# Kernel optimization log

Measured on AMD Instinct MI355X. Metric: run time of the kernel, lower is better.

Reference implementation:

```python
import jax, jax.numpy as jnp
import numpy as np

EPS = 1e-5
GROUPS = 8


def setup_inputs() -> dict:
    key = jax.random.key(0)
    ks = jax.random.split(key, 6)
    C = 512
    B, H, W = 4, 64, 64
    s = 1.0 / np.sqrt(C)
    return {
        "x": jax.random.normal(ks[0], (B, C, H, W), dtype=jnp.float32),
        "gn_gamma": jnp.ones((C,), jnp.float32),
        "gn_beta": jnp.zeros((C,), jnp.float32),
        "wq": jax.random.normal(ks[1], (C, C), jnp.float32) * s,
        "bq": jnp.zeros((C,), jnp.float32),
        "wk": jax.random.normal(ks[2], (C, C), jnp.float32) * s,
        "bk": jnp.zeros((C,), jnp.float32),
        "wv": jax.random.normal(ks[3], (C, C), jnp.float32) * s,
        "bv": jnp.zeros((C,), jnp.float32),
        "wp": jax.random.normal(ks[4], (C, C), jnp.float32) * s,
        "bp": jnp.zeros((C,), jnp.float32),
    }


def _group_norm(x, gamma, beta):
    b, c, h, w = x.shape
    xg = x.reshape(b, GROUPS, c // GROUPS, h, w)
    mu = xg.mean(axis=(2, 3, 4), keepdims=True)
    var = xg.var(axis=(2, 3, 4), keepdims=True)
    xn = ((xg - mu) * jax.lax.rsqrt(var + EPS)).reshape(b, c, h, w)
    return xn * gamma[None, :, None, None] + beta[None, :, None, None]


def _conv1x1(x, w, b):
    # 1x1 conv == channel-mixing matmul: [O,C] x [B,C,H,W] -> [B,O,H,W]
    return jnp.einsum('oc,bchw->bohw', w, x) + b[None, :, None, None]


def reference(x, gn_gamma, gn_beta, wq, bq, wk, bk, wv, bv, wp, bp):
    b, c, h, w = x.shape
    xn = _group_norm(x, gn_gamma, gn_beta)  # note: residual uses normalized x, as in source
    q = _conv1x1(xn, wq, bq).reshape(b, c, h * w)
    k = _conv1x1(xn, wk, bk).reshape(b, c, h * w)
    v = _conv1x1(xn, wv, bv).reshape(b, c, h * w)
    scale = jnp.asarray(c, x.dtype) ** 0.5
    attn = jnp.einsum('bci,bcj->bij', q, k) / scale  # [b, hw, hw]
    attn = jax.nn.softmax(attn, axis=2)
    out = jnp.einsum('bij,bcj->bci', attn, v).reshape(b, c, h, w)
    out = _conv1x1(out, wp, bp)
    return xn + out
```

## Files before the change

kernel.cpp:

```cpp
#include <hip/hip_runtime.h>
#include <hip/hip_bf16.h>


typedef unsigned short u16;
typedef unsigned char u8;
typedef __bf16 bf16x8 __attribute__((ext_vector_type(8)));
typedef float f32x4 __attribute__((ext_vector_type(4)));
typedef int i32x4 __attribute__((ext_vector_type(4)));
typedef int i32x8 __attribute__((ext_vector_type(8)));
typedef unsigned short u16x4 __attribute__((ext_vector_type(4)));
typedef unsigned short u16x8 __attribute__((ext_vector_type(8)));

#define CDIM 512
#define NPOS 4096
#define NBATCH 4

__device__ __forceinline__ u16 f2bf(float x) {
  union { float f; unsigned u; } c; c.f = x;
  unsigned u = c.u;
  u += 0x7fffu + ((u >> 16) & 1u);
  return (u16)(u >> 16);
}
__device__ __forceinline__ float bf2f(u16 h) {
  union { unsigned u; float f; } c; c.u = ((unsigned)h) << 16;
  return c.f;
}
__device__ __forceinline__ unsigned pk4_fp8(float a, float b, float c, float d) {
  unsigned v = __builtin_amdgcn_cvt_pk_fp8_f32(a, b, 0, false);
  v = __builtin_amdgcn_cvt_pk_fp8_f32(c, d, v, true);
  return v;
}

__device__ __forceinline__ void async16(const u16* g, u16* l) {
  __builtin_amdgcn_global_load_lds(
      (const __attribute__((address_space(1))) unsigned int*)g,
      (__attribute__((address_space(3))) unsigned int*)l, 16, 0, 0);
}
__device__ __forceinline__ void async16b(const u8* g, u8* l) {
  __builtin_amdgcn_global_load_lds(
      (const __attribute__((address_space(1))) unsigned int*)g,
      (__attribute__((address_space(3))) unsigned int*)l, 16, 0, 0);
}

__device__ __forceinline__ float wred_sum(float v) {
#pragma unroll
  for (int o = 32; o > 0; o >>= 1) v += __shfl_xor(v, o, 64);
  return v;
}

__global__ __launch_bounds__(256) void gn_partial(const float* __restrict__ x,
                                                  float* __restrict__ stats) {
  int gidx = blockIdx.x >> 3;
  int slice = blockIdx.x & 7;
  const float4* src = (const float4*)x + (long)gidx * 65536 + (long)slice * 8192;
  float s = 0.f, ss = 0.f;
  for (int i = threadIdx.x; i < 8192; i += 256) {
    float4 v = src[i];
    s  += v.x + v.y + v.z + v.w;
    ss += v.x * v.x + v.y * v.y + v.z * v.z + v.w * v.w;
  }
  s = wred_sum(s); ss = wred_sum(ss);
  __shared__ float r1[4], r2[4];
  int lane = threadIdx.x & 63, wave = threadIdx.x >> 6;
  if (lane == 0) { r1[wave] = s; r2[wave] = ss; }
  __syncthreads();
  if (threadIdx.x == 0) {
    atomicAdd(&stats[gidx * 2 + 0], r1[0] + r1[1] + r1[2] + r1[3]);
    atomicAdd(&stats[gidx * 2 + 1], r2[0] + r2[1] + r2[2] + r2[3]);
  }
}

__global__ __launch_bounds__(256) void norm_trans(const float* __restrict__ x,
                                                  const float* __restrict__ stats,
                                                  const float* __restrict__ gamma,
                                                  const float* __restrict__ beta,
                                                  u16* __restrict__ xnb,
                                                  u16* __restrict__ xnT) {
  __shared__ float tile[32][33];
  int b = blockIdx.z, c0 = blockIdx.y * 32, p0 = blockIdx.x * 32;
  int g = (b << 3) + (c0 >> 6);
  float cnt = 1.f / 262144.f;
  float mu = stats[g * 2 + 0] * cnt;
  float ms = stats[g * 2 + 1] * cnt;
  float rstd = rsqrtf(ms - mu * mu + 1e-5f);
  int tp = threadIdx.x & 31, tc = threadIdx.x >> 5;
#pragma unroll
  for (int r = 0; r < 4; r++) {
    int cl = tc + r * 8;
    int c = c0 + cl;
    long idx = ((long)(b * CDIM + c)) * NPOS + p0 + tp;
    float v = (x[idx] - mu) * rstd * gamma[c] + beta[c];
    xnb[idx] = f2bf(v);
    tile[cl][tp] = v;
  }
  __syncthreads();
#pragma unroll
  for (int r = 0; r < 4; r++) {
    int pl = tc + r * 8, cl = tp;
    xnT[((long)(b * NPOS + p0 + pl)) * CDIM + c0 + cl] = f2bf(tile[cl][pl]);
  }
}

__global__ __launch_bounds__(256) void cvt4(const float* __restrict__ a, const float* __restrict__ b,
                                            const float* __restrict__ c, const float* __restrict__ d,
                                            u16* __restrict__ oa, u16* __restrict__ ob,
                                            u16* __restrict__ oc, u16* __restrict__ od) {
  int i = blockIdx.x * 256 + threadIdx.x;
  if (blockIdx.y == 3) {
    int m = i >> 9, k = i & 511;
    u16 v = f2bf(d[i]);
    od[m * 1024 + k] = v;
    od[m * 1024 + 512 + k] = v;
    return;
  }
  const float* src; u16* dst;
  switch (blockIdx.y) {
    case 0: src = a; dst = oa; break;
    case 1: src = b; dst = ob; break;
    default: src = c; dst = oc; break;
  }
  dst[i] = f2bf(src[i]);
}

template <int MODE, int BN>
__global__ __launch_bounds__(BN * 2, 4) void gemm_bt(
    const u16* __restrict__ A, const u16* __restrict__ B,
    void* __restrict__ Cp, const float* __restrict__ bias,
    const float* __restrict__ bias1, const u16* __restrict__ residb,
    const float* __restrict__ laux,
    int N, int K, int lda, int ldb,
    long sA, long sB, long sC, long sR) {
  __shared__ u16 Asm[128 * 64];
  __shared__ u16 Bsm[BN * 64];
  constexpr int NT = BN * 2;
  constexpr int STEP = NT / 8;
  int bz = blockIdx.z;
  A += (long)bz * sA;
  B += (long)bz * sB;
  int bm = blockIdx.y, bn = blockIdx.x;
  int tid = threadIdx.x;
  int lane = tid & 63, wave = tid >> 6;
  int wm = (wave & 1) * 64, wn = (wave >> 1) * 64;

  int row0 = tid >> 3;
  int ko = (tid & 7) * 8;
  int kos = ko ^ ((row0 & 7) * 8);
  f32x4 acc[4][4] = {};
  int row16 = lane & 15;
  int kq = (lane >> 4) * 8;

  for (int k0 = 0; k0 < K; k0 += 64) {
#pragma unroll
    for (int r = 0; r < 128 / STEP; r++) {
      int row = row0 + r * STEP;
      async16(A + (long)(bm * 128 + row) * lda + k0 + kos, &Asm[row * 64 + ko]);
    }
#pragma unroll
    for (int r = 0; r < BN / STEP; r++) {
      int row = row0 + r * STEP;
      async16(B + (long)(bn * BN + row) * ldb + k0 + kos, &Bsm[row * 64 + ko]);
    }
    __syncthreads();
#pragma unroll
    for (int s2 = 0; s2 < 2; s2++) {
      bf16x8 af[4], bfr[4];
#pragma unroll
      for (int i = 0; i < 4; i++) {
        int row = wm + i * 16 + row16;
        af[i] = *(const bf16x8*)&Asm[row * 64 + ((s2 * 32 + kq) ^ ((row & 7) * 8))];
      }
#pragma unroll
      for (int j = 0; j < 4; j++) {
        int row = wn + j * 16 + row16;
        bfr[j] = *(const bf16x8*)&Bsm[row * 64 + ((s2 * 32 + kq) ^ ((row & 7) * 8))];
      }
#pragma unroll
      for (int i = 0; i < 4; i++)
#pragma unroll
        for (int j = 0; j < 4; j++)
          acc[i][j] = __builtin_amdgcn_mfma_f32_16x16x32_bf16(bfr[j], af[i], acc[i][j], 0, 0, 0);
    }
    __syncthreads();
  }

  int mcol = lane & 15, rb = (lane >> 4) * 4;
  long zC = (long)bz * sC;
#pragma unroll
  for (int i = 0; i < 4; i++) {
    int gm = bm * 128 + wm + i * 16 + mcol;
    float bm_add = 0.f;
    if constexpr (MODE == 4 || MODE == 5) bm_add = bias[gm];
#pragma unroll
    for (int j = 0; j < 4; j++) {
      int gn0 = bn * BN + wn + j * 16 + rb;
      long off = zC + (long)gm * N + gn0;
      float v[4];
#pragma unroll
      for (int r = 0; r < 4; r++) v[r] = acc[i][j][r];
      if constexpr (MODE == 0) {
        const float* bb = (gn0 < 512) ? (bias + gn0) : (bias1 + (gn0 - 512));
#pragma unroll
        for (int r = 0; r < 4; r++) v[r] += bb[r];
        *(unsigned*)&((u8*)Cp)[off] = pk4_fp8(v[0], v[1], v[2], v[3]);
      }
      if constexpr (MODE == 4) {
        f32x4 lv = *(const f32x4*)&laux[bz * NPOS + gn0];
        u16x4 rv = *(const u16x4*)&residb[(long)bz * sR + (long)gm * N + gn0];
        f32x4 o;
#pragma unroll
        for (int r = 0; r < 4; r++) o[r] = v[r] / lv[r] + bm_add + bf2f(rv[r]);
        *(f32x4*)&((float*)Cp)[off] = o;
      }
      if constexpr (MODE == 5) {
#pragma unroll
        for (int r = 0; r < 4; r++) v[r] += bm_add;
        *(unsigned*)&((u8*)Cp)[off] = pk4_fp8(v[0], v[1], v[2], v[3]);
      }
    }
  }
}

__global__ __launch_bounds__(256, 3) void smx_gemm(const u8* __restrict__ QKf8,
                                                   u8* __restrict__ P,
                                                   float* __restrict__ l,
                                                   float scale) {
  __shared__ u8 Asm[128 * 128];
  __shared__ u8 Bsm[128 * 128];
  int bz = blockIdx.z;
  const u8* Ab = QKf8 + (long)bz * 4194304;
  const u8* Bb = Ab + 512;
  int bm = blockIdx.y, bn = blockIdx.x;
  int tid = threadIdx.x, lane = tid & 63, wave = tid >> 6;
  int wm = (wave & 1) * 64, wn = (wave >> 1) * 64;
  int m16 = lane & 15, q = lane >> 4;
  int lrow8 = lane >> 3, lch = lane & 7;

  f32x4 acc[4][4] = {};

  for (int k0 = 0; k0 < 512; k0 += 128) {
#pragma unroll
    for (int r = 0; r < 4; r++) {
      int row = (wave * 4 + r) * 8 + lrow8;
      int ch = lch ^ (row & 7);
      async16b(Ab + (long)(bm * 128 + row) * 1024 + k0 + ch * 16, &Asm[row * 128 + lch * 16]);
      async16b(Bb + (long)(bn * 128 + row) * 1024 + k0 + ch * 16, &Bsm[row * 128 + lch * 16]);
    }
    __syncthreads();
    i32x8 af[4], bf[4];
#pragma unroll
    for (int i = 0; i < 4; i++) {
      int row = wm + i * 16 + m16;
      int sw = (row & 7) * 16;
      i32x4 lo = *(const i32x4*)&Asm[row * 128 + ((q * 32) ^ sw)];
      i32x4 hi = *(const i32x4*)&Asm[row * 128 + ((q * 32 + 16) ^ sw)];
      af[i] = __builtin_shufflevector(lo, hi, 0, 1, 2, 3, 4, 5, 6, 7);
    }
#pragma unroll
    for (int j = 0; j < 4; j++) {
      int row = wn + j * 16 + m16;
      int sw = (row & 7) * 16;
      i32x4 lo = *(const i32x4*)&Bsm[row * 128 + ((q * 32) ^ sw)];
      i32x4 hi = *(const i32x4*)&Bsm[row * 128 + ((q * 32 + 16) ^ sw)];
      bf[j] = __builtin_shufflevector(lo, hi, 0, 1, 2, 3, 4, 5, 6, 7);
    }
#pragma unroll
    for (int i = 0; i < 4; i++)
#pragma unroll
      for (int j = 0; j < 4; j++)
        acc[i][j] = __builtin_amdgcn_mfma_scale_f32_16x16x128_f8f6f4(
            bf[j], af[i], acc[i][j], 0, 0, 0, 0x7F7F7F7F, 0, 0x7F7F7F7F);
    __syncthreads();
  }

  long zC = (long)bz * 16777216;
  float rsum[4] = {0.f, 0.f, 0.f, 0.f};
#pragma unroll
  for (int i = 0; i < 4; i++) {
    int gi = bm * 128 + wm + i * 16 + m16;
#pragma unroll
    for (int j = 0; j < 4; j++) {
      int gj = bn * 128 + wn + j * 16 + q * 4;
      float v[4];
#pragma unroll
      for (int r = 0; r < 4; r++) { v[r] = __expf(acc[i][j][r] * scale); rsum[i] += v[r]; }
      *(unsigned*)&P[zC + (long)gi * 4096 + gj] = pk4_fp8(v[0], v[1], v[2], v[3]);
    }
  }
#pragma unroll
  for (int i = 0; i < 4; i++) {
    rsum[i] += __shfl_xor(rsum[i], 16, 64);
    rsum[i] += __shfl_xor(rsum[i], 32, 64);
  }
  if (lane < 16) {
    int base = bz * NPOS + bm * 128 + wm + m16;
#pragma unroll
    for (int i = 0; i < 4; i++)
      atomicAdd(&l[base + i * 16], rsum[i]);
  }
}

__global__ __launch_bounds__(256, 3) void hgemm_mx(const u8* __restrict__ P,
                                                   const u8* __restrict__ V,
                                                   u16* __restrict__ part) {
  __shared__ u8 Asm[128 * 128];
  __shared__ u8 Bsm[128 * 128];
  int z = blockIdx.z;
  int bz = z >> 1, sp = z & 1;
  const u8* Ab = P + (long)bz * 16777216 + sp * 2048;
  const u8* Bb = V + (long)bz * 2097152 + sp * 2048;
  int bm = blockIdx.y, bn = blockIdx.x;
  int tid = threadIdx.x, lane = tid & 63, wave = tid >> 6;
  int wm = (wave & 1) * 64, wn = (wave >> 1) * 64;
  int m16 = lane & 15, q = lane >> 4;
  int lrow8 = lane >> 3, lch = lane & 7;

  f32x4 acc[4][4] = {};

  for (int k0 = 0; k0 < 2048; k0 += 128) {
#pragma unroll
    for (int r = 0; r < 4; r++) {
      int row = (wave * 4 + r) * 8 + lrow8;
      int ch = lch ^ (row & 7);
      async16b(Ab + (long)(bm * 128 + row) * 4096 + k0 + ch * 16, &Asm[row * 128 + lch * 16]);
      async16b(Bb + (long)(bn * 128 + row) * 4096 + k0 + ch * 16, &Bsm[row * 128 + lch * 16]);
    }
    __syncthreads();
    i32x8 af[4], bf[4];
#pragma unroll
    for (int i = 0; i < 4; i++) {
      int row = wm + i * 16 + m16;
      int sw = (row & 7) * 16;
      i32x4 lo = *(const i32x4*)&Asm[row * 128 + ((q * 32) ^ sw)];
      i32x4 hi = *(const i32x4*)&Asm[row * 128 + ((q * 32 + 16) ^ sw)];
      af[i] = __builtin_shufflevector(lo, hi, 0, 1, 2, 3, 4, 5, 6, 7);
    }
#pragma unroll
    for (int j = 0; j < 4; j++) {
      int row = wn + j * 16 + m16;
      int sw = (row & 7) * 16;
      i32x4 lo = *(const i32x4*)&Bsm[row * 128 + ((q * 32) ^ sw)];
      i32x4 hi = *(const i32x4*)&Bsm[row * 128 + ((q * 32 + 16) ^ sw)];
      bf[j] = __builtin_shufflevector(lo, hi, 0, 1, 2, 3, 4, 5, 6, 7);
    }
#pragma unroll
    for (int i = 0; i < 4; i++)
#pragma unroll
      for (int j = 0; j < 4; j++)
        acc[i][j] = __builtin_amdgcn_mfma_scale_f32_16x16x128_f8f6f4(
            bf[j], af[i], acc[i][j], 0, 0, 0, 0x7F7F7F7F, 0, 0x7F7F7F7F);
    __syncthreads();
  }

  long zC = (long)bz * 4194304 + sp * 512;
#pragma unroll
  for (int i = 0; i < 4; i++) {
    int gi = bm * 128 + wm + i * 16 + m16;
#pragma unroll
    for (int j = 0; j < 4; j++) {
      int gc = bn * 128 + wn + j * 16 + q * 4;
      u16x4 o;
#pragma unroll
      for (int r = 0; r < 4; r++) o[r] = f2bf(acc[i][j][r]);
      *(u16x4*)&part[zC + (long)gi * 1024 + gc] = o;
    }
  }
}

extern "C" void kernel_launch(void* const* d_in, const int* in_sizes, int n_in,
                              void* d_out, int out_size, void* d_ws, size_t ws_size,
                              hipStream_t stream) {
  const float* x     = (const float*)d_in[0];
  const float* gamma = (const float*)d_in[1];
  const float* beta  = (const float*)d_in[2];
  const float* wq = (const float*)d_in[3];
  const float* bq = (const float*)d_in[4];
  const float* wk = (const float*)d_in[5];
  const float* bk = (const float*)d_in[6];
  const float* wv = (const float*)d_in[7];
  const float* bv = (const float*)d_in[8];
  const float* wp = (const float*)d_in[9];
  const float* bp = (const float*)d_in[10];
  float* out = (float*)d_out;

  char* W = (char*)d_ws;
  float* stats = (float*)(W + 0);
  float* l     = (float*)(W + 256);
  u16* xnb  = (u16*)(W + 65792);
  u16* xnT  = (u16*)(W + 16843008);
  u16* wqkb = (u16*)(W + 33620224);
  u16* wvb  = (u16*)(W + 34668800);
  u16* wpd  = (u16*)(W + 35193088);
  u8*  QKf8 = (u8*)(W + 37290240);
  u8*  Vf8  = (u8*)(W + 54067456);
  u16* part = (u16*)(W + 62456064);
  u8*  SP   = (u8*)(W + 96010496);
  (void)in_sizes; (void)n_in; (void)out_size; (void)ws_size;

  hipMemsetAsync(W, 0, 65792, stream);
  gn_partial<<<256, 256, 0, stream>>>(x, stats);
  norm_trans<<<dim3(128, 16, 4), 256, 0, stream>>>(x, stats, gamma, beta, xnb, xnT);
  cvt4<<<dim3(1024, 4), 256, 0, stream>>>(wq, wk, wv, wp, wqkb, wqkb + 262144, wvb, wpd);

  const long NC = (long)NPOS * CDIM;
  const long CN = (long)CDIM * NPOS;
  const long QKS = (long)NPOS * 1024;
  const float scale = 0.044194173824159216f;

  gemm_bt<0, 256><<<dim3(4, 128, 1), 512, 0, stream>>>(xnT, wqkb, QKf8, bq, bk, nullptr, nullptr,
      1024, CDIM, CDIM, CDIM, 0, 0, 0, 0);
  gemm_bt<5, 128><<<dim3(32, 4, 4), 256, 0, stream>>>(wvb, xnT, Vf8, bv, nullptr, nullptr, nullptr,
      NPOS, CDIM, CDIM, CDIM, 0, NC, CN, 0);
  smx_gemm<<<dim3(32, 32, NBATCH), 256, 0, stream>>>(QKf8, SP, l, scale);
  hgemm_mx<<<dim3(4, 32, 8), 256, 0, stream>>>(SP, Vf8, part);
  gemm_bt<4, 128><<<dim3(32, 4, 4), 256, 0, stream>>>(wpd, part, (void*)out, bp, nullptr, xnb, l,
      NPOS, 1024, 1024, 1024, 0, (long)NPOS * 1024, CN, CN);
}
```

Baseline: 326.9 us.

## Double-buffer LDS tiles in all GEMM kernels with prefetch and MFMA priority

Converts the bf16 gemm_bt, the fp8 score GEMM and the PV GEMM to double-buffered LDS. The next K tile is issued asynchronously before computing on the current one, and each step ends with an explicit vmcnt drain plus barrier. MFMA sections are wrapped in s_setprio to favour math issue. The QK projection launch also switches from a 256-wide tile to a 128-wide tile. Doubling LDS lowers the occupancy hint from 3-4 to 2 blocks per CU, which may reduce latency hiding.

```diff
diff --git a/kernel.cpp b/kernel.cpp
--- a/kernel.cpp
+++ b/kernel.cpp
@@ -40,6 +40,11 @@
   __builtin_amdgcn_global_load_lds(
       (const __attribute__((address_space(1))) unsigned int*)g,
       (__attribute__((address_space(3))) unsigned int*)l, 16, 0, 0);
+}
+
+__device__ __forceinline__ void drain_barrier() {
+  asm volatile("s_waitcnt vmcnt(0)" ::: "memory");
+  __builtin_amdgcn_s_barrier();
 }
 
 __device__ __forceinline__ float wred_sum(float v) {
@@ -123,15 +128,15 @@
 }
 
 template <int MODE, int BN>
-__global__ __launch_bounds__(BN * 2, 4) void gemm_bt(
+__global__ __launch_bounds__(BN * 2, 2) void gemm_bt(
     const u16* __restrict__ A, const u16* __restrict__ B,
     void* __restrict__ Cp, const float* __restrict__ bias,
     const float* __restrict__ bias1, const u16* __restrict__ residb,
     const float* __restrict__ laux,
     int N, int K, int lda, int ldb,
     long sA, long sB, long sC, long sR) {
-  __shared__ u16 Asm[128 * 64];
-  __shared__ u16 Bsm[BN * 64];
+  __shared__ u16 Asm[2][128 * 64];
+  __shared__ u16 Bsm[2][BN * 64];
   constexpr int NT = BN * 2;
   constexpr int STEP = NT / 8;
   int bz = blockIdx.z;
@@ -149,38 +154,47 @@
   int row16 = lane & 15;
   int kq = (lane >> 4) * 8;
 
-  for (int k0 = 0; k0 < K; k0 += 64) {
+  auto stage = [&](int buf, int k0) {
 #pragma unroll
     for (int r = 0; r < 128 / STEP; r++) {
       int row = row0 + r * STEP;
-      async16(A + (long)(bm * 128 + row) * lda + k0 + kos, &Asm[row * 64 + ko]);
+      async16(A + (long)(bm * 128 + row) * lda + k0 + kos, &Asm[buf][row * 64 + ko]);
     }
 #pragma unroll
     for (int r = 0; r < BN / STEP; r++) {
       int row = row0 + r * STEP;
-      async16(B + (long)(bn * BN + row) * ldb + k0 + kos, &Bsm[row * 64 + ko]);
-    }
-    __syncthreads();
+      async16(B + (long)(bn * BN + row) * ldb + k0 + kos, &Bsm[buf][row * 64 + ko]);
+    }
+  };
+
+  stage(0, 0);
+  drain_barrier();
+  int cur = 0;
+  for (int k0 = 0; k0 < K; k0 += 64) {
+    if (k0 + 64 < K) stage(cur ^ 1, k0 + 64);
 #pragma unroll
     for (int s2 = 0; s2 < 2; s2++) {
       bf16x8 af[4], bfr[4];
 #pragma unroll
       for (int i = 0; i < 4; i++) {
         int row = wm + i * 16 + row16;
-        af[i] = *(const bf16x8*)&Asm[row * 64 + ((s2 * 32 + kq) ^ ((row & 7) * 8))];
+        af[i] = *(const bf16x8*)&Asm[cur][row * 64 + ((s2 * 32 + kq) ^ ((row & 7) * 8))];
       }
 #pragma unroll
       for (int j = 0; j < 4; j++) {
         int row = wn + j * 16 + row16;
-        bfr[j] = *(const bf16x8*)&Bsm[row * 64 + ((s2 * 32 + kq) ^ ((row & 7) * 8))];
+        bfr[j] = *(const bf16x8*)&Bsm[cur][row * 64 + ((s2 * 32 + kq) ^ ((row & 7) * 8))];
       }
+      __builtin_amdgcn_s_setprio(1);
 #pragma unroll
       for (int i = 0; i < 4; i++)
 #pragma unroll
         for (int j = 0; j < 4; j++)
           acc[i][j] = __builtin_amdgcn_mfma_f32_16x16x32_bf16(bfr[j], af[i], acc[i][j], 0, 0, 0);
-    }
-    __syncthreads();
+      __builtin_amdgcn_s_setprio(0);
+    }
+    drain_barrier();
+    cur ^= 1;
   }
 
   int mcol = lane & 15, rb = (lane >> 4) * 4;
@@ -220,12 +234,12 @@
   }
 }
 
-__global__ __launch_bounds__(256, 3) void smx_gemm(const u8* __restrict__ QKf8,
+__global__ __launch_bounds__(256, 2) void smx_gemm(const u8* __restrict__ QKf8,
                                                    u8* __restrict__ P,
                                                    float* __restrict__ l,
                                                    float scale) {
-  __shared__ u8 Asm[128 * 128];
-  __shared__ u8 Bsm[128 * 128];
+  __shared__ u8 Asm[2][128 * 128];
+  __shared__ u8 Bsm[2][128 * 128];
   int bz = blockIdx.z;
   const u8* Ab = QKf8 + (long)bz * 4194304;
   const u8* Bb = Ab + 512;
@@ -237,39 +251,48 @@
 
   f32x4 acc[4][4] = {};
 
-  for (int k0 = 0; k0 < 512; k0 += 128) {
+  auto stage = [&](int buf, int k0) {
 #pragma unroll
     for (int r = 0; r < 4; r++) {
       int row = (wave * 4 + r) * 8 + lrow8;
       int ch = lch ^ (row & 7);
-      async16b(Ab + (long)(bm * 128 + row) * 1024 + k0 + ch * 16, &Asm[row * 128 + lch * 16]);
-      async16b(Bb + (long)(bn * 128 + row) * 1024 + k0 + ch * 16, &Bsm[row * 128 + lch * 16]);
-    }
-    __syncthreads();
+      async16b(Ab + (long)(bm * 128 + row) * 1024 + k0 + ch * 16, &Asm[buf][row * 128 + lch * 16]);
+      async16b(Bb + (long)(bn * 128 + row) * 1024 + k0 + ch * 16, &Bsm[buf][row * 128 + lch * 16]);
+    }
+  };
+
+  stage(0, 0);
+  drain_barrier();
+  int cur = 0;
+  for (int t = 0; t < 4; t++) {
+    if (t < 3) stage(cur ^ 1, (t + 1) * 128);
     i32x8 af[4], bf[4];
 #pragma unroll
     for (int i = 0; i < 4; i++) {
       int row = wm + i * 16 + m16;
       int sw = (row & 7) * 16;
-      i32x4 lo = *(const i32x4*)&Asm[row * 128 + ((q * 32) ^ sw)];
-      i32x4 hi = *(const i32x4*)&Asm[row * 128 + ((q * 32 + 16) ^ sw)];
+      i32x4 lo = *(const i32x4*)&Asm[cur][row * 128 + ((q * 32) ^ sw)];
+      i32x4 hi = *(const i32x4*)&Asm[cur][row * 128 + ((q * 32 + 16) ^ sw)];
       af[i] = __builtin_shufflevector(lo, hi, 0, 1, 2, 3, 4, 5, 6, 7);
     }
 #pragma unroll
     for (int j = 0; j < 4; j++) {
       int row = wn + j * 16 + m16;
       int sw = (row & 7) * 16;
-      i32x4 lo = *(const i32x4*)&Bsm[row * 128 + ((q * 32) ^ sw)];
-      i32x4 hi = *(const i32x4*)&Bsm[row * 128 + ((q * 32 + 16) ^ sw)];
+      i32x4 lo = *(const i32x4*)&Bsm[cur][row * 128 + ((q * 32) ^ sw)];
+      i32x4 hi = *(const i32x4*)&Bsm[cur][row * 128 + ((q * 32 + 16) ^ sw)];
       bf[j] = __builtin_shufflevector(lo, hi, 0, 1, 2, 3, 4, 5, 6, 7);
     }
+    __builtin_amdgcn_s_setprio(1);
 #pragma unroll
     for (int i = 0; i < 4; i++)
 #pragma unroll
       for (int j = 0; j < 4; j++)
         acc[i][j] = __builtin_amdgcn_mfma_scale_f32_16x16x128_f8f6f4(
             bf[j], af[i], acc[i][j], 0, 0, 0, 0x7F7F7F7F, 0, 0x7F7F7F7F);
-    __syncthreads();
+    __builtin_amdgcn_s_setprio(0);
+    drain_barrier();
+    cur ^= 1;
   }
 
   long zC = (long)bz * 16777216;
@@ -299,11 +322,11 @@
   }
 }
 
-__global__ __launch_bounds__(256, 3) void hgemm_mx(const u8* __restrict__ P,
+__global__ __launch_bounds__(256, 2) void hgemm_mx(const u8* __restrict__ P,
                                                    const u8* __restrict__ V,
                                                    u16* __restrict__ part) {
-  __shared__ u8 Asm[128 * 128];
-  __shared__ u8 Bsm[128 * 128];
+  __shared__ u8 Asm[2][128 * 128];
+  __shared__ u8 Bsm[2][128 * 128];
   int z = blockIdx.z;
   int bz = z >> 1, sp = z & 1;
   const u8* Ab = P + (long)bz * 16777216 + sp * 2048;
@@ -316,39 +339,48 @@
 
   f32x4 acc[4][4] = {};
 
-  for (int k0 = 0; k0 < 2048; k0 += 128) {
+  auto stage = [&](int buf, int k0) {
 #pragma unroll
     for (int r = 0; r < 4; r++) {
       int row = (wave * 4 + r) * 8 + lrow8;
       int ch = lch ^ (row & 7);
-      async16b(Ab + (long)(bm * 128 + row) * 4096 + k0 + ch * 16, &Asm[row * 128 + lch * 16]);
-      async16b(Bb + (long)(bn * 128 + row) * 4096 + k0 + ch * 16, &Bsm[row * 128 + lch * 16]);
-    }
-    __syncthreads();
+      async16b(Ab + (long)(bm * 128 + row) * 4096 + k0 + ch * 16, &Asm[buf][row * 128 + lch * 16]);
+      async16b(Bb + (long)(bn * 128 + row) * 4096 + k0 + ch * 16, &Bsm[buf][row * 128 + lch * 16]);
+    }
+  };
+
+  stage(0, 0);
+  drain_barrier();
+  int cur = 0;
+  for (int t = 0; t < 16; t++) {
+    if (t < 15) stage(cur ^ 1, (t + 1) * 128);
     i32x8 af[4], bf[4];
 #pragma unroll
     for (int i = 0; i < 4; i++) {
       int row = wm + i * 16 + m16;
       int sw = (row & 7) * 16;
-      i32x4 lo = *(const i32x4*)&Asm[row * 128 + ((q * 32) ^ sw)];
-      i32x4 hi = *(const i32x4*)&Asm[row * 128 + ((q * 32 + 16) ^ sw)];
+      i32x4 lo = *(const i32x4*)&Asm[cur][row * 128 + ((q * 32) ^ sw)];
+      i32x4 hi = *(const i32x4*)&Asm[cur][row * 128 + ((q * 32 + 16) ^ sw)];
       af[i] = __builtin_shufflevector(lo, hi, 0, 1, 2, 3, 4, 5, 6, 7);
     }
 #pragma unroll
     for (int j = 0; j < 4; j++) {
       int row = wn + j * 16 + m16;
       int sw = (row & 7) * 16;
-      i32x4 lo = *(const i32x4*)&Bsm[row * 128 + ((q * 32) ^ sw)];
-      i32x4 hi = *(const i32x4*)&Bsm[row * 128 + ((q * 32 + 16) ^ sw)];
+      i32x4 lo = *(const i32x4*)&Bsm[cur][row * 128 + ((q * 32) ^ sw)];
+      i32x4 hi = *(const i32x4*)&Bsm[cur][row * 128 + ((q * 32 + 16) ^ sw)];
       bf[j] = __builtin_shufflevector(lo, hi, 0, 1, 2, 3, 4, 5, 6, 7);
     }
+    __builtin_amdgcn_s_setprio(1);
 #pragma unroll
     for (int i = 0; i < 4; i++)
 #pragma unroll
       for (int j = 0; j < 4; j++)
         acc[i][j] = __builtin_amdgcn_mfma_scale_f32_16x16x128_f8f6f4(
             bf[j], af[i], acc[i][j], 0, 0, 0, 0x7F7F7F7F, 0, 0x7F7F7F7F);
-    __syncthreads();
+    __builtin_amdgcn_s_setprio(0);
+    drain_barrier();
+    cur ^= 1;
   }
 
   long zC = (long)bz * 4194304 + sp * 512;
@@ -403,10 +435,9 @@
 
   const long NC = (long)NPOS * CDIM;
   const long CN = (long)CDIM * NPOS;
-  const long QKS = (long)NPOS * 1024;
   const float scale = 0.044194173824159216f;
 
-  gemm_bt<0, 256><<<dim3(4, 128, 1), 512, 0, stream>>>(xnT, wqkb, QKf8, bq, bk, nullptr, nullptr,
+  gemm_bt<0, 128><<<dim3(8, 128, 1), 256, 0, stream>>>(xnT, wqkb, QKf8, bq, bk, nullptr, nullptr,
       1024, CDIM, CDIM, CDIM, 0, 0, 0, 0);
   gemm_bt<5, 128><<<dim3(32, 4, 4), 256, 0, stream>>>(wvb, xnT, Vf8, bv, nullptr, nullptr, nullptr,
       NPOS, CDIM, CDIM, CDIM, 0, NC, CN, 0);
```

Measured after the change: 322.4 us. Within noise of the previous version (-1.4%).
